# Optimization experiments

Measured on AMD Instinct MI355X. Metric: run time of the kernel, lower is better.

The kernel has to match this reference:

```python
import jax, jax.numpy as jnp
import numpy as np


def setup_inputs() -> dict:
    key = jax.random.key(0)
    ks = jax.random.split(key, 5)
    B, S, D, H = 2, 2048, 1024, 16
    dk = D // H
    scale = D ** -0.5
    x = jax.random.normal(ks[0], (B, S, D), dtype=jnp.float32)
    W_Q = scale * jax.random.normal(ks[1], (H, D, dk), dtype=jnp.float32)
    W_K = scale * jax.random.normal(ks[2], (H, D, dk), dtype=jnp.float32)
    W_V = scale * jax.random.normal(ks[3], (H, D, dk), dtype=jnp.float32)
    W_O = scale * jax.random.normal(ks[4], (H * dk, D), dtype=jnp.float32)
    return {"x": x, "W_Q": W_Q, "W_K": W_K, "W_V": W_V, "W_O": W_O}


def reference(x, W_Q, W_K, W_V, W_O):
    # x: [B,S,D]; W_Q/W_K/W_V: [H,D,dk]; W_O: [H*dk, D]
    dk = W_Q.shape[-1]
    Q = jnp.einsum('bsd,hdk->bhsk', x, W_Q)
    K = jnp.einsum('bsd,hdk->bhsk', x, W_K)
    V = jnp.einsum('bsd,hdk->bhsk', x, W_V)
    scores = jnp.einsum('bhqk,bhsk->bhqs', Q, K) / jnp.sqrt(jnp.float32(dk))
    attn = jax.nn.softmax(scores, axis=-1)
    heads = jnp.einsum('bhqs,bhsk->bhqk', attn, V)  # [B,H,S,dk]
    B, H, S, _ = heads.shape
    concat = heads.transpose(0, 2, 1, 3).reshape(B, S, H * dk)  # [B,S,H*dk]
    return concat @ W_O
```

## Files before the change

### kernel.cpp

```cpp
#include <hip/hip_runtime.h>

typedef __attribute__((ext_vector_type(8))) short bf16x8;
typedef __attribute__((ext_vector_type(4))) float f32x4;
typedef __attribute__((ext_vector_type(4))) unsigned short u16x4;
typedef unsigned short u16;
typedef unsigned int u32;

static __device__ __forceinline__ u16 f2bf(float f) {
  u32 u = __float_as_uint(f);
  u32 r = (u + 0x7fffu + ((u >> 16) & 1u)) >> 16;
  return (u16)r;
}

static __device__ __forceinline__ u32 cvt_pk(float lo, float hi) {
  u32 r;
  asm("v_cvt_pk_bf16_f32 %0, %1, %2" : "=v"(r) : "v"(lo), "v"(hi));
  return r;
}

#define GLDS16(g, l)                                                        \
  __builtin_amdgcn_global_load_lds(                                         \
      (const __attribute__((address_space(1))) u32*)(g),                    \
      (__attribute__((address_space(3))) u32*)(l), 16, 0, 0)

#define WAIT_VM3() asm volatile("s_waitcnt vmcnt(3)" ::: "memory")
#define WAIT_VM8() asm volatile("s_waitcnt vmcnt(8)" ::: "memory")
#define WAIT_VM0() asm volatile("s_waitcnt vmcnt(0)" ::: "memory")
#define RAWBAR() __builtin_amdgcn_s_barrier()

#define SC2F 0.18033688011112042f

__global__ __launch_bounds__(256) void cast_x(const float* __restrict__ x,
                                              u16* __restrict__ xb) {
  int i = blockIdx.x * 256 + threadIdx.x;
  const float4* xv = (const float4*)x;
  float4 a = xv[i * 2], b = xv[i * 2 + 1];
  bf16x8 o;
  o[0] = f2bf(a.x); o[1] = f2bf(a.y); o[2] = f2bf(a.z); o[3] = f2bf(a.w);
  o[4] = f2bf(b.x); o[5] = f2bf(b.y); o[6] = f2bf(b.z); o[7] = f2bf(b.w);
  *(bf16x8*)(xb + i * 8) = o;
}

__global__ __launch_bounds__(256) void cast_wqkv(const float* __restrict__ wq,
                                                 const float* __restrict__ wk,
                                                 const float* __restrict__ wv,
                                                 u16* __restrict__ wt) {
  __shared__ u16 tile[64][66];
  int bid = blockIdx.x;
  int dt = bid & 15, h = (bid >> 4) & 15, sel = bid >> 8;
  const float* src = (sel == 0 ? wq : (sel == 1 ? wk : wv)) + h * 65536 + dt * 4096;
  int t = threadIdx.x;
  int r = t >> 4, c4 = (t & 15) * 4;
#pragma unroll
  for (int p = 0; p < 4; ++p) {
    int rr = r + p * 16;
    float4 v = *(const float4*)(src + rr * 64 + c4);
    u16x4 o;
    o[0] = f2bf(v.x); o[1] = f2bf(v.y); o[2] = f2bf(v.z); o[3] = f2bf(v.w);
    *(u16x4*)&tile[rr][c4] = o;
  }
  __syncthreads();
  int kk = t >> 3, dc = (t & 7) * 8;
  u16* dstb = wt + ((size_t)(sel * 1024 + h * 64)) * 1024 + dt * 64;
#pragma unroll
  for (int p = 0; p < 2; ++p) {
    int kkp = kk + p * 32;
    u16x4 a, b2;
#pragma unroll
    for (int i = 0; i < 4; ++i) {
      a[i] = tile[dc + i][kkp];
      b2[i] = tile[dc + 4 + i][kkp];
    }
    *(u16x4*)(dstb + (size_t)kkp * 1024 + dc) = a;
    *(u16x4*)(dstb + (size_t)kkp * 1024 + dc + 4) = b2;
  }
}

__global__ __launch_bounds__(256) void cast_wo(const float* __restrict__ wo,
                                               u16* __restrict__ wt) {
  __shared__ u16 tile[64][66];
  int bid = blockIdx.x;
  int nt = bid & 15, kt = bid >> 4;
  const float* src = wo + (size_t)(kt * 64) * 1024 + nt * 64;
  int t = threadIdx.x;
  int r = t >> 4, c4 = (t & 15) * 4;
#pragma unroll
  for (int p = 0; p < 4; ++p) {
    int rr = r + p * 16;
    float4 v = *(const float4*)(src + (size_t)rr * 1024 + c4);
    u16x4 o;
    o[0] = f2bf(v.x); o[1] = f2bf(v.y); o[2] = f2bf(v.z); o[3] = f2bf(v.w);
    *(u16x4*)&tile[rr][c4] = o;
  }
  __syncthreads();
  int nn = t >> 3, dc = (t & 7) * 8;
  u16* dstb = wt + (size_t)(nt * 64) * 1024 + kt * 64;
#pragma unroll
  for (int p = 0; p < 2; ++p) {
    int np = nn + p * 32;
    u16x4 a, b2;
#pragma unroll
    for (int i = 0; i < 4; ++i) {
      a[i] = tile[dc + i][np];
      b2[i] = tile[dc + 4 + i][np];
    }
    *(u16x4*)(dstb + (size_t)np * 1024 + dc) = a;
    *(u16x4*)(dstb + (size_t)np * 1024 + dc + 4) = b2;
  }
}

__global__ __launch_bounds__(512) void gemm_qkv(const u16* __restrict__ A,
                                                const u16* __restrict__ Bt,
                                                u16* __restrict__ qkb,
                                                u16* __restrict__ Vt, int M,
                                                int N, int K) {
  const int t = threadIdx.x;
  const int lane = t & 63, w = t >> 6;
  const int lr = lane & 15, lg = lane >> 4;
  const int wr = w >> 1, wc = w & 1;
  int lin = blockIdx.y * gridDim.x + blockIdx.x;
  int nwg = gridDim.x * gridDim.y;
  int swz = (lin & 7) * (nwg >> 3) + (lin >> 3);
  int bx = swz % gridDim.x, by = swz / gridDim.x;
  const int m0 = by * 256, n0 = bx * 128;
  __shared__ __align__(16) u16 SM[24576];
  const int ra = t >> 2, ca = (t & 3) * 8;
  const u16* a0 = A + (size_t)(m0 + ra) * K + ca;
  const u16* b0 = Bt + (size_t)(n0 + ra) * K + ca;
  const size_t ajmp = (size_t)128 * K;
  f32x4 acc[4][4] = {};

#define QSTAGE(bb, k0)                                       \
  {                                                          \
    GLDS16(a0 + (k0), &SM[(bb)*8192 + t * 8]);               \
    GLDS16(a0 + ajmp + (k0), &SM[(bb)*8192 + 4096 + t * 8]); \
    GLDS16(b0 + (k0), &SM[16384 + (bb)*4096 + t * 8]);       \
  }

  QSTAGE(0, 0);
  for (int k0 = 0; k0 < K; k0 += 32) {
    const int bb = (k0 >> 5) & 1;
    if (k0 + 32 < K) {
      QSTAGE(bb ^ 1, k0 + 32);
      WAIT_VM3();
    } else {
      WAIT_VM0();
    }
    RAWBAR();
    bf16x8 a[4], b[4];
#pragma unroll
    for (int m = 0; m < 4; ++m)
      a[m] = *(const bf16x8*)&SM[bb * 8192 + (wr * 64 + m * 16 + lr) * 32 + lg * 8];
#pragma unroll
    for (int n = 0; n < 4; ++n)
      b[n] = *(const bf16x8*)&SM[16384 + bb * 4096 + (wc * 64 + n * 16 + lr) * 32 + lg * 8];
    __builtin_amdgcn_s_setprio(1);
#pragma unroll
    for (int m = 0; m < 4; ++m)
#pragma unroll
      for (int n = 0; n < 4; ++n)
        acc[m][n] =
            __builtin_amdgcn_mfma_f32_16x16x32_bf16(a[m], b[n], acc[m][n], 0, 0, 0);
    __builtin_amdgcn_s_setprio(0);
    RAWBAR();
  }
#undef QSTAGE

  if (n0 < 2048) {
#pragma unroll
    for (int m = 0; m < 4; ++m) {
      int rowg = m0 + wr * 64 + m * 16 + lg * 4;
#pragma unroll
      for (int n = 0; n < 4; ++n) {
        int colg = n0 + wc * 64 + n * 16 + lr;
        float sc = colg < 1024 ? SC2F : 1.0f;
#pragma unroll
        for (int j = 0; j < 4; ++j)
          qkb[(size_t)(rowg + j) * 2048 + colg] = f2bf(acc[m][n][j] * sc);
      }
    }
  } else {
    const int bb2 = m0 >> 11, s0g = m0 & 2047;
    const int vbase = n0 - 2048;
#pragma unroll
    for (int c = 0; c < 2; ++c) {
      __syncthreads();
      if ((wr >> 1) == c) {
#pragma unroll
        for (int m = 0; m < 4; ++m)
#pragma unroll
          for (int n = 0; n < 4; ++n) {
            u16x4 pk;
#pragma unroll
            for (int j = 0; j < 4; ++j) pk[j] = f2bf(acc[m][n][j]);
            int vidx = wc * 64 + n * 16 + lr;
            int sl = (wr & 1) * 64 + m * 16 + lg * 4;
            *(u16x4*)&SM[vidx * 136 + sl] = pk;
          }
      }
      __syncthreads();
#pragma unroll
      for (int q = 0; q < 4; ++q) {
        int id = q * 512 + t;
        int vv = id >> 4, sc = id & 15;
        bf16x8 row = *(const bf16x8*)&SM[vv * 136 + sc * 8];
        *(bf16x8*)(Vt + ((size_t)(bb2 * 1024 + vbase + vv)) * 2048 + s0g +
                   c * 128 + sc * 8) = row;
      }
    }
  }
}

__global__ __launch_bounds__(256) void gemm_out(const u16* __restrict__ A,
                                                const u16* __restrict__ Bt,
                                                float* __restrict__ C, int M,
                                                int N, int K) {
  const int t = threadIdx.x;
  const int lane = t & 63, w = t >> 6;
  const int lr = lane & 15, lg = lane >> 4;
  const int wr = w >> 1, wc = w & 1;
  int lin = blockIdx.y * gridDim.x + blockIdx.x;
  int nwg = gridDim.x * gridDim.y;
  int swz = (lin & 7) * (nwg >> 3) + (lin >> 3);
  int bx = swz % gridDim.x, by = swz / gridDim.x;
  const int m0 = by * 128, n0 = bx * 128;
  __shared__ __align__(16) u16 As[2][128 * 32];
  __shared__ __align__(16) u16 Bs[2][128 * 32];
  const int r0 = t >> 2, cb = (t & 3) * 8;
  const u16* a0 = A + (size_t)(m0 + r0) * K + cb;
  const u16* b0 = Bt + (size_t)(n0 + r0) * K + cb;
  const size_t rowjmp = (size_t)64 * K;
  f32x4 acc[4][4] = {};

#define GSTAGE(bb, k0)                                      \
  {                                                         \
    GLDS16(a0 + (k0), &As[bb][t * 8]);                      \
    GLDS16(a0 + rowjmp + (k0), &As[bb][2048 + t * 8]);      \
    GLDS16(b0 + (k0), &Bs[bb][t * 8]);                      \
    GLDS16(b0 + rowjmp + (k0), &Bs[bb][2048 + t * 8]);      \
  }

  GSTAGE(0, 0);
  for (int k0 = 0; k0 < K; k0 += 32) {
    const int bb = (k0 >> 5) & 1;
    if (k0 + 32 < K) {
      GSTAGE(bb ^ 1, k0 + 32);
      asm volatile("s_waitcnt vmcnt(4)" ::: "memory");
    } else {
      WAIT_VM0();
    }
    RAWBAR();
    bf16x8 a[4], b[4];
#pragma unroll
    for (int m = 0; m < 4; ++m)
      a[m] = *(const bf16x8*)&As[bb][(wr * 64 + m * 16 + lr) * 32 + lg * 8];
#pragma unroll
    for (int n = 0; n < 4; ++n)
      b[n] = *(const bf16x8*)&Bs[bb][(wc * 64 + n * 16 + lr) * 32 + lg * 8];
    __builtin_amdgcn_s_setprio(1);
#pragma unroll
    for (int m = 0; m < 4; ++m)
#pragma unroll
      for (int n = 0; n < 4; ++n)
        acc[m][n] =
            __builtin_amdgcn_mfma_f32_16x16x32_bf16(a[m], b[n], acc[m][n], 0, 0, 0);
    __builtin_amdgcn_s_setprio(0);
    RAWBAR();
  }
#undef GSTAGE

#pragma unroll
  for (int m = 0; m < 4; ++m) {
    int rowg = m0 + wr * 64 + m * 16 + lg * 4;
#pragma unroll
    for (int n = 0; n < 4; ++n) {
      int colg = n0 + wc * 64 + n * 16 + lr;
#pragma unroll
      for (int j = 0; j < 4; ++j)
        C[(size_t)(rowg + j) * N + colg] = acc[m][n][j];
    }
  }
}

__global__ __launch_bounds__(256, 2) void attn(const u16* __restrict__ qkb,
                                               const u16* __restrict__ vtb,
                                               u16* __restrict__ hb) {
  const int t = threadIdx.x, lane = t & 63, w = t >> 6;
  const int lr = lane & 15, lg = lane >> 4;
  int lin = blockIdx.x;
  int swz2 = (lin & 7) * 64 + (lin >> 3);
  int qi = swz2 & 15, bh = swz2 >> 4;
  int b = bh >> 4, h = bh & 15;
  int q0 = qi * 128;
  __shared__ __align__(16) u16 Ks[2][128 * 64];
  __shared__ __align__(16) u16 Vts[2][64 * 128];
  __shared__ __align__(16) u32 Ps[4][2][512];

  bf16x8 qf[2][2];
#pragma unroll
  for (int g = 0; g < 2; ++g) {
    const u16* qb =
        qkb + (size_t)(b * 2048 + q0 + w * 32 + g * 16 + lr) * 2048 + h * 64;
    qf[g][0] = *(const bf16x8*)(qb + lg * 8);
    qf[g][1] = *(const bf16x8*)(qb + 32 + lg * 8);
  }

  f32x4 oacc[2][4] = {};
  float mrun0 = -1e30f, mrun1 = -1e30f;
  float lrun0 = 0.f, lrun1 = 0.f;

  int chk[2], chv[4];
#pragma unroll
  for (int kk = 0; kk < 2; ++kk) chk[kk] = ((kk * 4 + lg) ^ (lr & 7)) * 8;
#pragma unroll
  for (int kk = 0; kk < 4; ++kk) chv[kk] = ((kk * 4 + lg) ^ lr) * 8;
  const int xw = (lr & 7) << 2;

  const int rk = t >> 3, ck = t & 7;
  const int rv = t >> 4, cv = t & 15;
  const u16* Kg = qkb + (size_t)(b * 2048) * 2048 + 1024 + h * 64;
  const u16* Vg = vtb + (size_t)(b * 1024 + h * 64) * 2048;
  const u16* kp0 = Kg + (size_t)rk * 2048 + ((ck ^ (rk & 7)) * 8);
  const u16* vp0 = Vg + (size_t)rv * 2048 + ((cv ^ (rv & 15)) * 8);
  u32* Pw0 = &Ps[w][0][0];
  u32* Pw1 = &Ps[w][1][0];

#define ASTAGE(bb, tv)                                 \
  {                                                    \
    const u16* kp = kp0 + (size_t)(tv)*262144;         \
    const u16* vp = vp0 + (tv)*128;                    \
    GLDS16(kp, &Ks[bb][t * 8]);                        \
    GLDS16(kp + 65536, &Ks[bb][2048 + t * 8]);         \
    GLDS16(kp + 131072, &Ks[bb][4096 + t * 8]);        \
    GLDS16(kp + 196608, &Ks[bb][6144 + t * 8]);        \
    GLDS16(vp, &Vts[bb][t * 8]);                       \
    GLDS16(vp + 32768, &Vts[bb][2048 + t * 8]);        \
    GLDS16(vp + 65536, &Vts[bb][4096 + t * 8]);        \
    GLDS16(vp + 98304, &Vts[bb][6144 + t * 8]);        \
  }

  ASTAGE(0, 0);
  for (int tv = 0; tv < 16; ++tv) {
    const int bb = tv & 1;
    if (tv < 15) {
      ASTAGE(bb ^ 1, tv + 1);
      WAIT_VM8();
    } else {
      WAIT_VM0();
    }
    RAWBAR();

    f32x4 s0[8], s1[8];
#pragma unroll
    for (int n = 0; n < 8; ++n) {
      s0[n] = (f32x4){0.f, 0.f, 0.f, 0.f};
      s1[n] = (f32x4){0.f, 0.f, 0.f, 0.f};
    }
    __builtin_amdgcn_s_setprio(1);
#pragma unroll
    for (int kk = 0; kk < 2; ++kk)
#pragma unroll
      for (int n = 0; n < 8; ++n) {
        bf16x8 kf = *(const bf16x8*)&Ks[bb][n * 1024 + lr * 64 + chk[kk]];
        s0[n] = __builtin_amdgcn_mfma_f32_16x16x32_bf16(kf, qf[0][kk], s0[n], 0, 0, 0);
        s1[n] = __builtin_amdgcn_mfma_f32_16x16x32_bf16(kf, qf[1][kk], s1[n], 0, 0, 0);
      }
    __builtin_amdgcn_s_setprio(0);

    float t0[8], t1[8];
#pragma unroll
    for (int n = 0; n < 8; ++n) {
      t0[n] = fmaxf(fmaxf(s0[n][0], s0[n][1]), fmaxf(s0[n][2], s0[n][3]));
      t1[n] = fmaxf(fmaxf(s1[n][0], s1[n][1]), fmaxf(s1[n][2], s1[n][3]));
    }
    float pm0 = fmaxf(fmaxf(fmaxf(t0[0], t0[1]), fmaxf(t0[2], t0[3])),
                      fmaxf(fmaxf(t0[4], t0[5]), fmaxf(t0[6], t0[7])));
    float pm1 = fmaxf(fmaxf(fmaxf(t1[0], t1[1]), fmaxf(t1[2], t1[3])),
                      fmaxf(fmaxf(t1[4], t1[5]), fmaxf(t1[6], t1[7])));
    pm0 = fmaxf(pm0, __shfl_xor(pm0, 16));
    pm0 = fmaxf(pm0, __shfl_xor(pm0, 32));
    pm1 = fmaxf(pm1, __shfl_xor(pm1, 16));
    pm1 = fmaxf(pm1, __shfl_xor(pm1, 32));

    if (__any(fmaxf(pm0 - mrun0, pm1 - mrun1) > 8.0f)) {
      {
        float mn = fmaxf(mrun0, pm0);
        float al = __builtin_amdgcn_exp2f(mrun0 - mn);
        lrun0 *= al;
        float alj[4];
#pragma unroll
        for (int j = 0; j < 4; ++j) alj[j] = __shfl(al, 4 * lg + j);
#pragma unroll
        for (int n = 0; n < 4; ++n)
#pragma unroll
          for (int j = 0; j < 4; ++j) oacc[0][n][j] *= alj[j];
        mrun0 = mn;
      }
      {
        float mn = fmaxf(mrun1, pm1);
        float al = __builtin_amdgcn_exp2f(mrun1 - mn);
        lrun1 *= al;
        float alj[4];
#pragma unroll
        for (int j = 0; j < 4; ++j) alj[j] = __shfl(al, 4 * lg + j);
#pragma unroll
        for (int n = 0; n < 4; ++n)
#pragma unroll
          for (int j = 0; j < 4; ++j) oacc[1][n][j] *= alj[j];
        mrun1 = mn;
      }
    }

    float ps0 = 0.f, ps1 = 0.f;
#pragma unroll
    for (int n = 0; n < 4; ++n) {
      float v0 = __builtin_amdgcn_exp2f(s0[n][0] - mrun0);
      float v1 = __builtin_amdgcn_exp2f(s0[n][1] - mrun0);
      float v2 = __builtin_amdgcn_exp2f(s0[n][2] - mrun0);
      float v3 = __builtin_amdgcn_exp2f(s0[n][3] - mrun0);
      ps0 += (v0 + v1) + (v2 + v3);
      Pw0[lr * 32 + ((8 * n + 2 * lg) ^ xw)] = cvt_pk(v0, v1);
      Pw0[lr * 32 + ((8 * n + 2 * lg + 1) ^ xw)] = cvt_pk(v2, v3);
      float u0 = __builtin_amdgcn_exp2f(s1[n][0] - mrun1);
      float u1 = __builtin_amdgcn_exp2f(s1[n][1] - mrun1);
      float u2 = __builtin_amdgcn_exp2f(s1[n][2] - mrun1);
      float u3 = __builtin_amdgcn_exp2f(s1[n][3] - mrun1);
      ps1 += (u0 + u1) + (u2 + u3);
      Pw1[lr * 32 + ((8 * n + 2 * lg) ^ xw)] = cvt_pk(u0, u1);
      Pw1[lr * 32 + ((8 * n + 2 * lg + 1) ^ xw)] = cvt_pk(u2, u3);
    }
    __builtin_amdgcn_s_setprio(1);
#pragma unroll
    for (int kk = 0; kk < 2; ++kk) {
      bf16x8 pa0 = *(const bf16x8*)&Pw0[lr * 32 + ((16 * kk + 4 * lg) ^ xw)];
      bf16x8 pa1 = *(const bf16x8*)&Pw1[lr * 32 + ((16 * kk + 4 * lg) ^ xw)];
#pragma unroll
      for (int n = 0; n < 4; ++n) {
        bf16x8 vf = *(const bf16x8*)&Vts[bb][n * 2048 + lr * 128 + chv[kk]];
        oacc[0][n] = __builtin_amdgcn_mfma_f32_16x16x32_bf16(pa0, vf, oacc[0][n], 0, 0, 0);
        oacc[1][n] = __builtin_amdgcn_mfma_f32_16x16x32_bf16(pa1, vf, oacc[1][n], 0, 0, 0);
      }
    }
    __builtin_amdgcn_s_setprio(0);
#pragma unroll
    for (int n = 4; n < 8; ++n) {
      float v0 = __builtin_amdgcn_exp2f(s0[n][0] - mrun0);
      float v1 = __builtin_amdgcn_exp2f(s0[n][1] - mrun0);
      float v2 = __builtin_amdgcn_exp2f(s0[n][2] - mrun0);
      float v3 = __builtin_amdgcn_exp2f(s0[n][3] - mrun0);
      ps0 += (v0 + v1) + (v2 + v3);
      Pw0[lr * 32 + ((8 * (n - 4) + 2 * lg) ^ xw)] = cvt_pk(v0, v1);
      Pw0[lr * 32 + ((8 * (n - 4) + 2 * lg + 1) ^ xw)] = cvt_pk(v2, v3);
      float u0 = __builtin_amdgcn_exp2f(s1[n][0] - mrun1);
      float u1 = __builtin_amdgcn_exp2f(s1[n][1] - mrun1);
      float u2 = __builtin_amdgcn_exp2f(s1[n][2] - mrun1);
      float u3 = __builtin_amdgcn_exp2f(s1[n][3] - mrun1);
      ps1 += (u0 + u1) + (u2 + u3);
      Pw1[lr * 32 + ((8 * (n - 4) + 2 * lg) ^ xw)] = cvt_pk(u0, u1);
      Pw1[lr * 32 + ((8 * (n - 4) + 2 * lg + 1) ^ xw)] = cvt_pk(u2, u3);
    }
    __builtin_amdgcn_s_setprio(1);
#pragma unroll
    for (int kk = 2; kk < 4; ++kk) {
      bf16x8 pa0 = *(const bf16x8*)&Pw0[lr * 32 + ((16 * (kk - 2) + 4 * lg) ^ xw)];
      bf16x8 pa1 = *(const bf16x8*)&Pw1[lr * 32 + ((16 * (kk - 2) + 4 * lg) ^ xw)];
#pragma unroll
      for (int n = 0; n < 4; ++n) {
        bf16x8 vf = *(const bf16x8*)&Vts[bb][n * 2048 + lr * 128 + chv[kk]];
        oacc[0][n] = __builtin_amdgcn_mfma_f32_16x16x32_bf16(pa0, vf, oacc[0][n], 0, 0, 0);
        oacc[1][n] = __builtin_amdgcn_mfma_f32_16x16x32_bf16(pa1, vf, oacc[1][n], 0, 0, 0);
      }
    }
    __builtin_amdgcn_s_setprio(0);
    lrun0 += ps0;
    lrun1 += ps1;
    RAWBAR();
  }
#undef ASTAGE

  lrun0 += __shfl_xor(lrun0, 16);
  lrun0 += __shfl_xor(lrun0, 32);
  lrun1 += __shfl_xor(lrun1, 16);
  lrun1 += __shfl_xor(lrun1, 32);
  float ri0 = __builtin_amdgcn_rcpf(lrun0);
  float ri1 = __builtin_amdgcn_rcpf(lrun1);
  float rj0[4], rj1[4];
#pragma unroll
  for (int j = 0; j < 4; ++j) {
    rj0[j] = __shfl(ri0, 4 * lg + j);
    rj1[j] = __shfl(ri1, 4 * lg + j);
  }
  int row0 = b * 2048 + q0 + w * 32 + lg * 4;
#pragma unroll
  for (int n = 0; n < 4; ++n) {
    int col = h * 64 + n * 16 + lr;
#pragma unroll
    for (int j = 0; j < 4; ++j) {
      hb[(size_t)(row0 + j) * 1024 + col] = f2bf(oacc[0][n][j] * rj0[j]);
      hb[(size_t)(row0 + 16 + j) * 1024 + col] = f2bf(oacc[1][n][j] * rj1[j]);
    }
  }
}

extern "C" void kernel_launch(void* const* d_in, const int* in_sizes, int n_in,
                              void* d_out, int out_size, void* d_ws,
                              size_t ws_size, hipStream_t stream) {
  const float* x = (const float*)d_in[0];
  const float* wq = (const float*)d_in[1];
  const float* wk = (const float*)d_in[2];
  const float* wv = (const float*)d_in[3];
  const float* wo = (const float*)d_in[4];

  u16* xb = (u16*)d_ws;
  u16* wqkv = xb + 4 * 1024 * 1024;
  u16* wot = wqkv + 3 * 1024 * 1024;
  u16* qkb = wot + 1024 * 1024;
  u16* vtb = qkb + 8 * 1024 * 1024;
  u16* hb = vtb + 4 * 1024 * 1024;

  cast_x<<<2048, 256, 0, stream>>>(x, xb);
  cast_wqkv<<<768, 256, 0, stream>>>(wq, wk, wv, wqkv);
  cast_wo<<<256, 256, 0, stream>>>(wo, wot);
  gemm_qkv<<<dim3(24, 16), 512, 0, stream>>>(xb, wqkv, qkb, vtb, 4096, 3072, 1024);
  attn<<<512, 256, 0, stream>>>(qkb, vtb, hb);
  gemm_out<<<dim3(8, 32), 256, 0, stream>>>(hb, wot, (float*)d_out, 4096, 1024, 1024);
}
```

Measured before the change: 127.3 us.

## Fuse cast kernels and retile QKV GEMM per head with interleaved weights

Merges the three fp32-to-bf16 cast kernels into one launch, and reorders the QKV weight layout so each head's Q, K, V columns sit together. The QKV GEMM now uses 128x192 tiles with 256 threads, so each block covers exactly one head's Q, K and V and writes all three, with V going out transposed through LDS. The goals are to cut launch overhead, remove the divergent split between QK blocks and V blocks, and give the GEMM more blocks (512 instead of 384). The smaller M tile lowers reuse of the weight operand, and in wave column 1 a third of the accumulator tiles hold both K and V columns, which unbalances the store work.

```diff
diff --git a/kernel.cpp b/kernel.cpp
--- a/kernel.cpp
+++ b/kernel.cpp
@@ -23,78 +23,67 @@
       (const __attribute__((address_space(1))) u32*)(g),                    \
       (__attribute__((address_space(3))) u32*)(l), 16, 0, 0)
 
-#define WAIT_VM3() asm volatile("s_waitcnt vmcnt(3)" ::: "memory")
+#define WAIT_VM5() asm volatile("s_waitcnt vmcnt(5)" ::: "memory")
 #define WAIT_VM8() asm volatile("s_waitcnt vmcnt(8)" ::: "memory")
+#define WAIT_VM4() asm volatile("s_waitcnt vmcnt(4)" ::: "memory")
 #define WAIT_VM0() asm volatile("s_waitcnt vmcnt(0)" ::: "memory")
 #define RAWBAR() __builtin_amdgcn_s_barrier()
 
 #define SC2F 0.18033688011112042f
 
-__global__ __launch_bounds__(256) void cast_x(const float* __restrict__ x,
-                                              u16* __restrict__ xb) {
-  int i = blockIdx.x * 256 + threadIdx.x;
-  const float4* xv = (const float4*)x;
-  float4 a = xv[i * 2], b = xv[i * 2 + 1];
-  bf16x8 o;
-  o[0] = f2bf(a.x); o[1] = f2bf(a.y); o[2] = f2bf(a.z); o[3] = f2bf(a.w);
-  o[4] = f2bf(b.x); o[5] = f2bf(b.y); o[6] = f2bf(b.z); o[7] = f2bf(b.w);
-  *(bf16x8*)(xb + i * 8) = o;
-}
-
-__global__ __launch_bounds__(256) void cast_wqkv(const float* __restrict__ wq,
-                                                 const float* __restrict__ wk,
-                                                 const float* __restrict__ wv,
-                                                 u16* __restrict__ wt) {
+__global__ __launch_bounds__(256) void cast_all(const float* __restrict__ x,
+                                                const float* __restrict__ wq,
+                                                const float* __restrict__ wk,
+                                                const float* __restrict__ wv,
+                                                const float* __restrict__ wo,
+                                                u16* __restrict__ xb,
+                                                u16* __restrict__ wqkv,
+                                                u16* __restrict__ wot) {
   __shared__ u16 tile[64][66];
-  int bid = blockIdx.x;
-  int dt = bid & 15, h = (bid >> 4) & 15, sel = bid >> 8;
-  const float* src = (sel == 0 ? wq : (sel == 1 ? wk : wv)) + h * 65536 + dt * 4096;
-  int t = threadIdx.x;
-  int r = t >> 4, c4 = (t & 15) * 4;
-#pragma unroll
-  for (int p = 0; p < 4; ++p) {
-    int rr = r + p * 16;
-    float4 v = *(const float4*)(src + rr * 64 + c4);
-    u16x4 o;
-    o[0] = f2bf(v.x); o[1] = f2bf(v.y); o[2] = f2bf(v.z); o[3] = f2bf(v.w);
-    *(u16x4*)&tile[rr][c4] = o;
-  }
-  __syncthreads();
-  int kk = t >> 3, dc = (t & 7) * 8;
-  u16* dstb = wt + ((size_t)(sel * 1024 + h * 64)) * 1024 + dt * 64;
-#pragma unroll
-  for (int p = 0; p < 2; ++p) {
-    int kkp = kk + p * 32;
-    u16x4 a, b2;
-#pragma unroll
-    for (int i = 0; i < 4; ++i) {
-      a[i] = tile[dc + i][kkp];
-      b2[i] = tile[dc + 4 + i][kkp];
-    }
-    *(u16x4*)(dstb + (size_t)kkp * 1024 + dc) = a;
-    *(u16x4*)(dstb + (size_t)kkp * 1024 + dc + 4) = b2;
-  }
-}
-
-__global__ __launch_bounds__(256) void cast_wo(const float* __restrict__ wo,
-                                               u16* __restrict__ wt) {
-  __shared__ u16 tile[64][66];
-  int bid = blockIdx.x;
-  int nt = bid & 15, kt = bid >> 4;
-  const float* src = wo + (size_t)(kt * 64) * 1024 + nt * 64;
-  int t = threadIdx.x;
-  int r = t >> 4, c4 = (t & 15) * 4;
-#pragma unroll
-  for (int p = 0; p < 4; ++p) {
-    int rr = r + p * 16;
-    float4 v = *(const float4*)(src + (size_t)rr * 1024 + c4);
-    u16x4 o;
-    o[0] = f2bf(v.x); o[1] = f2bf(v.y); o[2] = f2bf(v.z); o[3] = f2bf(v.w);
-    *(u16x4*)&tile[rr][c4] = o;
+  int bid = blockIdx.x, t = threadIdx.x;
+  if (bid < 2048) {
+    int i = bid * 256 + t;
+    const float4* xv = (const float4*)x;
+    float4 a = xv[i * 2], b = xv[i * 2 + 1];
+    bf16x8 o;
+    o[0] = f2bf(a.x); o[1] = f2bf(a.y); o[2] = f2bf(a.z); o[3] = f2bf(a.w);
+    o[4] = f2bf(b.x); o[5] = f2bf(b.y); o[6] = f2bf(b.z); o[7] = f2bf(b.w);
+    *(bf16x8*)(xb + i * 8) = o;
+    return;
+  }
+  const float* src;
+  u16* dstb;
+  if (bid < 2816) {
+    int id = bid - 2048;
+    int dt = id & 15, h = (id >> 4) & 15, sel = id >> 8;
+    src = (sel == 0 ? wq : (sel == 1 ? wk : wv)) + h * 65536 + dt * 4096;
+    dstb = wqkv + ((size_t)(h * 192 + sel * 64)) * 1024 + dt * 64;
+    int r = t >> 4, c4 = (t & 15) * 4;
+#pragma unroll
+    for (int p = 0; p < 4; ++p) {
+      int rr = r + p * 16;
+      float4 v = *(const float4*)(src + rr * 64 + c4);
+      u16x4 o;
+      o[0] = f2bf(v.x); o[1] = f2bf(v.y); o[2] = f2bf(v.z); o[3] = f2bf(v.w);
+      *(u16x4*)&tile[rr][c4] = o;
+    }
+  } else {
+    int id = bid - 2816;
+    int nt = id & 15, kt = id >> 4;
+    src = wo + (size_t)(kt * 64) * 1024 + nt * 64;
+    dstb = wot + (size_t)(nt * 64) * 1024 + kt * 64;
+    int r = t >> 4, c4 = (t & 15) * 4;
+#pragma unroll
+    for (int p = 0; p < 4; ++p) {
+      int rr = r + p * 16;
+      float4 v = *(const float4*)(src + (size_t)rr * 1024 + c4);
+      u16x4 o;
+      o[0] = f2bf(v.x); o[1] = f2bf(v.y); o[2] = f2bf(v.z); o[3] = f2bf(v.w);
+      *(u16x4*)&tile[rr][c4] = o;
+    }
   }
   __syncthreads();
   int nn = t >> 3, dc = (t & 7) * 8;
-  u16* dstb = wt + (size_t)(nt * 64) * 1024 + kt * 64;
 #pragma unroll
   for (int p = 0; p < 2; ++p) {
     int np = nn + p * 32;
@@ -109,7 +98,7 @@
   }
 }
 
-__global__ __launch_bounds__(512) void gemm_qkv(const u16* __restrict__ A,
+__global__ __launch_bounds__(256) void gemm_qkv(const u16* __restrict__ A,
                                                 const u16* __restrict__ Bt,
                                                 u16* __restrict__ qkb,
                                                 u16* __restrict__ Vt, int M,
@@ -122,19 +111,20 @@
   int nwg = gridDim.x * gridDim.y;
   int swz = (lin & 7) * (nwg >> 3) + (lin >> 3);
   int bx = swz % gridDim.x, by = swz / gridDim.x;
-  const int m0 = by * 256, n0 = bx * 128;
-  __shared__ __align__(16) u16 SM[24576];
+  const int m0 = by * 128, n0 = bx * 192, head = bx;
+  __shared__ __align__(16) u16 SM[20480];
   const int ra = t >> 2, ca = (t & 3) * 8;
   const u16* a0 = A + (size_t)(m0 + ra) * K + ca;
   const u16* b0 = Bt + (size_t)(n0 + ra) * K + ca;
-  const size_t ajmp = (size_t)128 * K;
-  f32x4 acc[4][4] = {};
-
-#define QSTAGE(bb, k0)                                       \
-  {                                                          \
-    GLDS16(a0 + (k0), &SM[(bb)*8192 + t * 8]);               \
-    GLDS16(a0 + ajmp + (k0), &SM[(bb)*8192 + 4096 + t * 8]); \
-    GLDS16(b0 + (k0), &SM[16384 + (bb)*4096 + t * 8]);       \
+  f32x4 acc[4][6] = {};
+
+#define QSTAGE(bb, k0)                                              \
+  {                                                                 \
+    GLDS16(a0 + (k0), &SM[(bb)*4096 + t * 8]);                      \
+    GLDS16(a0 + (size_t)64 * K + (k0), &SM[(bb)*4096 + 2048 + t * 8]); \
+    GLDS16(b0 + (k0), &SM[8192 + (bb)*6144 + t * 8]);               \
+    GLDS16(b0 + (size_t)64 * K + (k0), &SM[8192 + (bb)*6144 + 2048 + t * 8]); \
+    GLDS16(b0 + (size_t)128 * K + (k0), &SM[8192 + (bb)*6144 + 4096 + t * 8]); \
   }
 
   QSTAGE(0, 0);
@@ -142,23 +132,23 @@
     const int bb = (k0 >> 5) & 1;
     if (k0 + 32 < K) {
       QSTAGE(bb ^ 1, k0 + 32);
-      WAIT_VM3();
+      WAIT_VM5();
     } else {
       WAIT_VM0();
     }
     RAWBAR();
-    bf16x8 a[4], b[4];
+    bf16x8 a[4], b[6];
 #pragma unroll
     for (int m = 0; m < 4; ++m)
-      a[m] = *(const bf16x8*)&SM[bb * 8192 + (wr * 64 + m * 16 + lr) * 32 + lg * 8];
-#pragma unroll
-    for (int n = 0; n < 4; ++n)
-      b[n] = *(const bf16x8*)&SM[16384 + bb * 4096 + (wc * 64 + n * 16 + lr) * 32 + lg * 8];
+      a[m] = *(const bf16x8*)&SM[bb * 4096 + (wr * 64 + m * 16 + lr) * 32 + lg * 8];
+#pragma unroll
+    for (int n = 0; n < 6; ++n)
+      b[n] = *(const bf16x8*)&SM[8192 + bb * 6144 + (wc * 96 + n * 16 + lr) * 32 + lg * 8];
     __builtin_amdgcn_s_setprio(1);
 #pragma unroll
     for (int m = 0; m < 4; ++m)
 #pragma unroll
-      for (int n = 0; n < 4; ++n)
+      for (int n = 0; n < 6; ++n)
         acc[m][n] =
             __builtin_amdgcn_mfma_f32_16x16x32_bf16(a[m], b[n], acc[m][n], 0, 0, 0);
     __builtin_amdgcn_s_setprio(0);
@@ -166,48 +156,48 @@
   }
 #undef QSTAGE
 
-  if (n0 < 2048) {
-#pragma unroll
-    for (int m = 0; m < 4; ++m) {
-      int rowg = m0 + wr * 64 + m * 16 + lg * 4;
-#pragma unroll
-      for (int n = 0; n < 4; ++n) {
-        int colg = n0 + wc * 64 + n * 16 + lr;
-        float sc = colg < 1024 ? SC2F : 1.0f;
+#pragma unroll
+  for (int m = 0; m < 4; ++m) {
+    int rowg = m0 + wr * 64 + m * 16 + lg * 4;
+#pragma unroll
+    for (int n = 0; n < 6; ++n) {
+      int cg = wc * 96 + n * 16 + lr;
+      if (cg < 64) {
+        int col = head * 64 + cg;
 #pragma unroll
         for (int j = 0; j < 4; ++j)
-          qkb[(size_t)(rowg + j) * 2048 + colg] = f2bf(acc[m][n][j] * sc);
-      }
-    }
-  } else {
-    const int bb2 = m0 >> 11, s0g = m0 & 2047;
-    const int vbase = n0 - 2048;
-#pragma unroll
-    for (int c = 0; c < 2; ++c) {
-      __syncthreads();
-      if ((wr >> 1) == c) {
-#pragma unroll
-        for (int m = 0; m < 4; ++m)
-#pragma unroll
-          for (int n = 0; n < 4; ++n) {
-            u16x4 pk;
-#pragma unroll
-            for (int j = 0; j < 4; ++j) pk[j] = f2bf(acc[m][n][j]);
-            int vidx = wc * 64 + n * 16 + lr;
-            int sl = (wr & 1) * 64 + m * 16 + lg * 4;
-            *(u16x4*)&SM[vidx * 136 + sl] = pk;
-          }
-      }
-      __syncthreads();
-#pragma unroll
-      for (int q = 0; q < 4; ++q) {
-        int id = q * 512 + t;
-        int vv = id >> 4, sc = id & 15;
-        bf16x8 row = *(const bf16x8*)&SM[vv * 136 + sc * 8];
-        *(bf16x8*)(Vt + ((size_t)(bb2 * 1024 + vbase + vv)) * 2048 + s0g +
-                   c * 128 + sc * 8) = row;
-      }
-    }
+          qkb[(size_t)(rowg + j) * 2048 + col] = f2bf(acc[m][n][j] * SC2F);
+      } else if (cg < 128) {
+        int col = 1024 + head * 64 + (cg - 64);
+#pragma unroll
+        for (int j = 0; j < 4; ++j)
+          qkb[(size_t)(rowg + j) * 2048 + col] = f2bf(acc[m][n][j]);
+      }
+    }
+  }
+  __syncthreads();
+  if (wc == 1) {
+#pragma unroll
+    for (int m = 0; m < 4; ++m)
+#pragma unroll
+      for (int n = 2; n < 6; ++n) {
+        int v = (n - 2) * 16 + lr;
+        int s = wr * 64 + m * 16 + lg * 4;
+        u16x4 pk;
+#pragma unroll
+        for (int j = 0; j < 4; ++j) pk[j] = f2bf(acc[m][n][j]);
+        *(u16x4*)&SM[v * 136 + s] = pk;
+      }
+  }
+  __syncthreads();
+  const int bb2 = m0 >> 11, s0g = m0 & 2047;
+  u16* vdst = Vt + ((size_t)(bb2 * 1024 + head * 64)) * 2048 + s0g;
+#pragma unroll
+  for (int q = 0; q < 4; ++q) {
+    int id = q * 256 + t;
+    int v = id >> 4, sc = id & 15;
+    bf16x8 row = *(const bf16x8*)&SM[v * 136 + sc * 8];
+    *(bf16x8*)(vdst + (size_t)v * 2048 + sc * 8) = row;
   }
 }
 
@@ -245,7 +235,7 @@
     const int bb = (k0 >> 5) & 1;
     if (k0 + 32 < K) {
       GSTAGE(bb ^ 1, k0 + 32);
-      asm volatile("s_waitcnt vmcnt(4)" ::: "memory");
+      WAIT_VM4();
     } else {
       WAIT_VM0();
     }
@@ -518,10 +508,8 @@
   u16* vtb = qkb + 8 * 1024 * 1024;
   u16* hb = vtb + 4 * 1024 * 1024;
 
-  cast_x<<<2048, 256, 0, stream>>>(x, xb);
-  cast_wqkv<<<768, 256, 0, stream>>>(wq, wk, wv, wqkv);
-  cast_wo<<<256, 256, 0, stream>>>(wo, wot);
-  gemm_qkv<<<dim3(24, 16), 512, 0, stream>>>(xb, wqkv, qkb, vtb, 4096, 3072, 1024);
+  cast_all<<<3072, 256, 0, stream>>>(x, wq, wk, wv, wo, xb, wqkv, wot);
+  gemm_qkv<<<dim3(16, 32), 256, 0, stream>>>(xb, wqkv, qkb, vtb, 4096, 3072, 1024);
   attn<<<512, 256, 0, stream>>>(qkb, vtb, hb);
   gemm_out<<<dim3(8, 32), 256, 0, stream>>>(hb, wot, (float*)d_out, 4096, 1024, 1024);
 }
```

Measured after the change: 123.3 us. -3.1%, faster.
